# Kernel tuning notes

Hardware: AMD Instinct MI355X
Metric: run time of the kernel (lower is better)

Reference implementation:

```python
import jax, jax.numpy as jnp
import numpy as np

DIM = 768
NUM_HEADS = 12
HEAD_DIM = DIM // NUM_HEADS
ORDER_H = 8
RENORM = True
B, N = 4, 1024


def setup_inputs() -> dict:
    key = jax.random.key(0)
    ks = jax.random.split(key, 8)
    return {
        "x": jax.random.normal(ks[0], (B, N, DIM), dtype=jnp.float32),
        "qkv_w": jax.random.normal(ks[1], (3 * DIM, DIM), dtype=jnp.float32) * (DIM ** -0.5),
        "qkv_b": jax.random.normal(ks[2], (3 * DIM,), dtype=jnp.float32) * 0.02,
        "proj_w": jax.random.normal(ks[3], (DIM, DIM), dtype=jnp.float32) * (DIM ** -0.5),
        "proj_b": jax.random.normal(ks[4], (DIM,), dtype=jnp.float32) * 0.02,
        "lamb": jax.random.normal(ks[5], (NUM_HEADS,), dtype=jnp.float32) * 0.1,
        "gamma": 1.0 + jax.random.normal(ks[6], (NUM_HEADS,), dtype=jnp.float32) * 0.1,
        "delta": jax.random.normal(ks[7], (NUM_HEADS,), dtype=jnp.float32) * 0.1,
    }


def reference(x, qkv_w, qkv_b, proj_w, proj_b, lamb, gamma, delta):
    Bx, Nx, C = x.shape
    scale = HEAD_DIM ** -0.5
    # qkv: [B,N,3C] -> [3,B,H,N,hd]
    qkv = (x @ qkv_w.T + qkv_b).reshape(Bx, Nx, 3, NUM_HEADS, HEAD_DIM)
    qkv = jnp.transpose(qkv, (2, 0, 3, 1, 4))
    q, k, v = qkv[0], qkv[1], qkv[2]
    attn = jax.nn.softmax(jnp.einsum("bhid,bhjd->bhij", q, k) * scale, axis=-1)
    I = jnp.eye(Nx, dtype=attn.dtype)
    # GFSA high-order term: (h-1)*(A - I)@A + A
    high = (ORDER_H - 1) * jnp.einsum("bhik,bhkj->bhij", attn - I, attn) + attn
    beta_ = lamb[None, :, None, None]
    gamma_ = gamma[None, :, None, None]
    delta_ = delta[None, :, None, None]
    attn = delta_ * I + gamma_ * attn + beta_ * high
    if RENORM:
        attn = jnp.maximum(attn, 0.0)
        attn = attn / (attn.sum(axis=-1, keepdims=True) + 1e-9)
    out = jnp.einsum("bhij,bhjd->bhid", attn, v)  # [B,H,N,hd]
    out = jnp.transpose(out, (0, 2, 1, 3)).reshape(Bx, Nx, C)
    return out @ proj_w.T + proj_b
```

## Files before the change

### kernel.cpp

```cpp
#include <hip/hip_runtime.h>
#include <hip/hip_bf16.h>

#define DIMC 768
#define NH 12
#define HD 64
#define BB 4
#define NN 1024
#define BHT 48
#define QKVC 2304

typedef unsigned short u16;
typedef __attribute__((ext_vector_type(4))) unsigned short u16x4;
typedef __attribute__((ext_vector_type(8))) unsigned short u16x8;
typedef __attribute__((ext_vector_type(8))) short s16x8;
typedef __attribute__((ext_vector_type(4))) float f32x4;

#define GLD16(g, l) __builtin_amdgcn_global_load_lds( \
    (__attribute__((address_space(1))) void*)(g),     \
    (__attribute__((address_space(3))) void*)(l), 16, 0, 0)

__device__ __forceinline__ u16 f2bf(float f) {
    unsigned u = __float_as_uint(f);
    return (u16)((u + 0x7FFF + ((u >> 16) & 1)) >> 16);
}
__device__ __forceinline__ float bf2f(u16 v) {
    return __uint_as_float(((unsigned)v) << 16);
}
struct bfp { u16 h, l; };
__device__ __forceinline__ bfp splitf(float f) {
    bfp r;
    r.h = f2bf(f);
    r.l = f2bf(f - bf2f(r.h));
    return r;
}

__device__ __forceinline__ int swz_linear() {
    const int nwg = gridDim.x * gridDim.y * gridDim.z;
    const int L = blockIdx.x + gridDim.x * (blockIdx.y + gridDim.y * blockIdx.z);
    return (L & 7) * (nwg >> 3) + (L >> 3);
}

__global__ __launch_bounds__(256) void split_f2b(
    const float* __restrict__ src, u16* __restrict__ hi, u16* __restrict__ lo,
    int n4)
{
    int idx = blockIdx.x * 256 + threadIdx.x;
    if (idx >= n4) return;
    float4 v = *(const float4*)&src[idx * 4];
    u16x4 h, l;
    bfp s;
    s = splitf(v.x); h[0] = s.h; l[0] = s.l;
    s = splitf(v.y); h[1] = s.h; l[1] = s.l;
    s = splitf(v.z); h[2] = s.h; l[2] = s.l;
    s = splitf(v.w); h[3] = s.h; l[3] = s.l;
    *(u16x4*)&hi[idx * 4] = h;
    *(u16x4*)&lo[idx * 4] = l;
}

__global__ __launch_bounds__(256, 3) void gemm3_mfma(
    int Mrows, int Nout, int K,
    const u16* __restrict__ Ahp, const u16* __restrict__ Alp,
    const u16* __restrict__ Bhp, const u16* __restrict__ Blp,
    const float* __restrict__ bias, float* __restrict__ C)
{
    __shared__ alignas(16) u16 sAh[128 * 32], sAl[128 * 32], sBh[128 * 32], sBl[128 * 32];
    const int tid = threadIdx.x;
    const int W = swz_linear();
    const int j0 = (W % gridDim.x) * 128, i0 = (W / gridDim.x) * 128;
    const int w = tid >> 6, l = tid & 63;
    const int wr = w >> 1, wc = w & 1;
    const int l15 = l & 15, kb4 = l >> 4;
    const int lrow = l >> 2, lch = (l & 3) * 8;

    f32x4 acc[4][4];
    const f32x4 zero = {0.f, 0.f, 0.f, 0.f};
#pragma unroll
    for (int a = 0; a < 4; ++a)
#pragma unroll
        for (int b = 0; b < 4; ++b) acc[a][b] = zero;

    for (int k0 = 0; k0 < K; k0 += 32) {
#pragma unroll
        for (int t = 0; t < 2; ++t) {
            const int r = w * 32 + t * 16;
            const size_t ar = (size_t)(i0 + r + lrow) * K + k0 + lch;
            const size_t br = (size_t)(j0 + r + lrow) * K + k0 + lch;
            GLD16(&Ahp[ar], &sAh[r * 32]);
            GLD16(&Alp[ar], &sAl[r * 32]);
            GLD16(&Bhp[br], &sBh[r * 32]);
            GLD16(&Blp[br], &sBl[r * 32]);
        }
        __syncthreads();

        s16x8 ah[4], al[4], bh[4], bl[4];
#pragma unroll
        for (int f = 0; f < 4; ++f) {
            const int ao = (wr * 64 + f * 16 + l15) * 32 + kb4 * 8;
            const int bo = (wc * 64 + f * 16 + l15) * 32 + kb4 * 8;
            ah[f] = *(const s16x8*)&sAh[ao];
            al[f] = *(const s16x8*)&sAl[ao];
            bh[f] = *(const s16x8*)&sBh[bo];
            bl[f] = *(const s16x8*)&sBl[bo];
        }
#pragma unroll
        for (int fr = 0; fr < 4; ++fr)
#pragma unroll
            for (int fc = 0; fc < 4; ++fc) {
                acc[fr][fc] = __builtin_amdgcn_mfma_f32_16x16x32_bf16(
                    ah[fr], bh[fc], acc[fr][fc], 0, 0, 0);
                acc[fr][fc] = __builtin_amdgcn_mfma_f32_16x16x32_bf16(
                    ah[fr], bl[fc], acc[fr][fc], 0, 0, 0);
                acc[fr][fc] = __builtin_amdgcn_mfma_f32_16x16x32_bf16(
                    al[fr], bh[fc], acc[fr][fc], 0, 0, 0);
            }
        __syncthreads();
    }

#pragma unroll
    for (int fr = 0; fr < 4; ++fr)
#pragma unroll
        for (int r = 0; r < 4; ++r) {
            const int gi = i0 + wr * 64 + fr * 16 + kb4 * 4 + r;
#pragma unroll
            for (int fc = 0; fc < 4; ++fc) {
                const int gj = j0 + wc * 64 + fc * 16 + l15;
                C[(size_t)gi * Nout + gj] = acc[fr][fc][r] + bias[gj];
            }
        }
}

__global__ __launch_bounds__(256, 3) void qkv_fused_mfma(
    const u16* __restrict__ Ahp, const u16* __restrict__ Alp,
    const u16* __restrict__ Bhp, const u16* __restrict__ Blp,
    const float* __restrict__ bias,
    u16* __restrict__ qh, u16* __restrict__ ql,
    u16* __restrict__ kh, u16* __restrict__ kl,
    u16* __restrict__ vth, u16* __restrict__ vtl)
{
    __shared__ alignas(16) u16 sAh[128 * 32], sAl[128 * 32], sBh[128 * 32], sBl[128 * 32];
    const int tid = threadIdx.x;
    const int W = swz_linear();
    const int j0 = (W % gridDim.x) * 128, i0 = (W / gridDim.x) * 128;
    const int w = tid >> 6, l = tid & 63;
    const int wr = w >> 1, wc = w & 1;
    const int l15 = l & 15, kb4 = l >> 4;
    const int lrow = l >> 2, lch = (l & 3) * 8;
    const int K = DIMC;

    f32x4 acc[4][4];
    const f32x4 zero = {0.f, 0.f, 0.f, 0.f};
#pragma unroll
    for (int a = 0; a < 4; ++a)
#pragma unroll
        for (int b = 0; b < 4; ++b) acc[a][b] = zero;

    for (int k0 = 0; k0 < K; k0 += 32) {
#pragma unroll
        for (int t = 0; t < 2; ++t) {
            const int r = w * 32 + t * 16;
            const size_t ar = (size_t)(i0 + r + lrow) * K + k0 + lch;
            const size_t br = (size_t)(j0 + r + lrow) * K + k0 + lch;
            GLD16(&Ahp[ar], &sAh[r * 32]);
            GLD16(&Alp[ar], &sAl[r * 32]);
            GLD16(&Bhp[br], &sBh[r * 32]);
            GLD16(&Blp[br], &sBl[r * 32]);
        }
        __syncthreads();

        s16x8 ah[4], al[4], bh[4], bl[4];
#pragma unroll
        for (int f = 0; f < 4; ++f) {
            const int ao = (wr * 64 + f * 16 + l15) * 32 + kb4 * 8;
            const int bo = (wc * 64 + f * 16 + l15) * 32 + kb4 * 8;
            ah[f] = *(const s16x8*)&sAh[ao];
            al[f] = *(const s16x8*)&sAl[ao];
            bh[f] = *(const s16x8*)&sBh[bo];
            bl[f] = *(const s16x8*)&sBl[bo];
        }
#pragma unroll
        for (int fr = 0; fr < 4; ++fr)
#pragma unroll
            for (int fc = 0; fc < 4; ++fc) {
                acc[fr][fc] = __builtin_amdgcn_mfma_f32_16x16x32_bf16(
                    ah[fr], bh[fc], acc[fr][fc], 0, 0, 0);
                acc[fr][fc] = __builtin_amdgcn_mfma_f32_16x16x32_bf16(
                    ah[fr], bl[fc], acc[fr][fc], 0, 0, 0);
                acc[fr][fc] = __builtin_amdgcn_mfma_f32_16x16x32_bf16(
                    al[fr], bh[fc], acc[fr][fc], 0, 0, 0);
            }
        __syncthreads();
    }

    const int part = j0 / DIMC;
    const int hbase = (j0 % DIMC) >> 6;
    const int h = hbase + wc;

#pragma unroll
    for (int fr = 0; fr < 4; ++fr) {
        const int rowbase = i0 + wr * 64 + fr * 16 + kb4 * 4;
        const int b = rowbase >> 10;
        const int n0 = rowbase & 1023;
        const int bh = b * NH + h;
#pragma unroll
        for (int fc = 0; fc < 4; ++fc) {
            const int gj = j0 + wc * 64 + fc * 16 + l15;
            const float bv = bias[gj];
            const int d = fc * 16 + l15;
            if (part == 0) {
#pragma unroll
                for (int r = 0; r < 4; ++r) {
                    bfp s = splitf((acc[fr][fc][r] + bv) * 0.125f);
                    const size_t o = ((size_t)bh * NN + n0 + r) * HD + d;
                    qh[o] = s.h; ql[o] = s.l;
                }
            } else if (part == 1) {
#pragma unroll
                for (int r = 0; r < 4; ++r) {
                    bfp s = splitf(acc[fr][fc][r] + bv);
                    const size_t o = ((size_t)bh * NN + n0 + r) * HD + d;
                    kh[o] = s.h; kl[o] = s.l;
                }
            } else {
                u16x4 hv, lv;
#pragma unroll
                for (int r = 0; r < 4; ++r) {
                    bfp s = splitf(acc[fr][fc][r] + bv);
                    hv[r] = s.h; lv[r] = s.l;
                }
                const size_t o = ((size_t)bh * HD + d) * NN + n0;
                *(u16x4*)&vth[o] = hv;
                *(u16x4*)&vtl[o] = lv;
            }
        }
    }
}

__global__ __launch_bounds__(256, 4) void qk_mfma(
    const u16* __restrict__ qh, const u16* __restrict__ ql,
    const u16* __restrict__ kh, const u16* __restrict__ kl,
    float* __restrict__ Sb, int h0)
{
    __shared__ alignas(16) u16 sAh[128 * 32], sAl[128 * 32], sBh[128 * 32], sBl[128 * 32];
    const int tid = threadIdx.x;
    const int W = swz_linear();
    const int bhl = W >> 6;
    const int ib = W & 63;
    const int j0 = (ib & 7) * 128, i0 = (ib >> 3) * 128;
    const int bh = h0 + bhl;
    const int w = tid >> 6, l = tid & 63;
    const int wr = w >> 1, wc = w & 1;
    const int l15 = l & 15, kb4 = l >> 4;
    const int lrow = l >> 2, lch = (l & 3) * 8;

    f32x4 acc[4][4];
    const f32x4 zero = {0.f, 0.f, 0.f, 0.f};
#pragma unroll
    for (int a = 0; a < 4; ++a)
#pragma unroll
        for (int b = 0; b < 4; ++b) acc[a][b] = zero;

    for (int k0 = 0; k0 < HD; k0 += 32) {
#pragma unroll
        for (int t = 0; t < 2; ++t) {
            const int r = w * 32 + t * 16;
            const size_t ar = ((size_t)bh * NN + i0 + r + lrow) * HD + k0 + lch;
            const size_t br = ((size_t)bh * NN + j0 + r + lrow) * HD + k0 + lch;
            GLD16(&qh[ar], &sAh[r * 32]);
            GLD16(&ql[ar], &sAl[r * 32]);
            GLD16(&kh[br], &sBh[r * 32]);
            GLD16(&kl[br], &sBl[r * 32]);
        }
        __syncthreads();

        s16x8 ah[4], al[4], bh[4], bl[4];
#pragma unroll
        for (int f = 0; f < 4; ++f) {
            const int ao = (wr * 64 + f * 16 + l15) * 32 + kb4 * 8;
            const int bo = (wc * 64 + f * 16 + l15) * 32 + kb4 * 8;
            ah[f] = *(const s16x8*)&sAh[ao];
            al[f] = *(const s16x8*)&sAl[ao];
            bh[f] = *(const s16x8*)&sBh[bo];
            bl[f] = *(const s16x8*)&sBl[bo];
        }
#pragma unroll
        for (int fr = 0; fr < 4; ++fr)
#pragma unroll
            for (int fc = 0; fc < 4; ++fc) {
                acc[fr][fc] = __builtin_amdgcn_mfma_f32_16x16x32_bf16(
                    ah[fr], bh[fc], acc[fr][fc], 0, 0, 0);
                acc[fr][fc] = __builtin_amdgcn_mfma_f32_16x16x32_bf16(
                    ah[fr], bl[fc], acc[fr][fc], 0, 0, 0);
                acc[fr][fc] = __builtin_amdgcn_mfma_f32_16x16x32_bf16(
                    al[fr], bh[fc], acc[fr][fc], 0, 0, 0);
            }
        __syncthreads();
    }

    float* Sh = Sb + (size_t)bhl * NN * NN;
#pragma unroll
    for (int fr = 0; fr < 4; ++fr)
#pragma unroll
        for (int r = 0; r < 4; ++r) {
            const int gi = i0 + wr * 64 + fr * 16 + kb4 * 4 + r;
#pragma unroll
            for (int fc = 0; fc < 4; ++fc) {
                const int gj = j0 + wc * 64 + fc * 16 + l15;
                Sh[(size_t)gi * NN + gj] = acc[fr][fc][r];
            }
        }
}

__global__ __launch_bounds__(256) void softmax_w(
    const float* __restrict__ Sb, u16* __restrict__ Abf)
{
    const int w = threadIdx.x >> 6, l = threadIdx.x & 63;
    const int row = blockIdx.x * 4 + w;
    const float* p = Sb + (size_t)row * NN;
    u16* q = Abf + (size_t)row * NN;

    float4 v[4];
    float m = -1e30f;
#pragma unroll
    for (int c = 0; c < 4; ++c) {
        v[c] = *(const float4*)&p[c * 256 + l * 4];
        m = fmaxf(m, fmaxf(fmaxf(v[c].x, v[c].y), fmaxf(v[c].z, v[c].w)));
    }
#pragma unroll
    for (int off = 32; off >= 1; off >>= 1) m = fmaxf(m, __shfl_xor(m, off));

    float s = 0.f;
#pragma unroll
    for (int c = 0; c < 4; ++c) {
        v[c].x = expf(v[c].x - m); v[c].y = expf(v[c].y - m);
        v[c].z = expf(v[c].z - m); v[c].w = expf(v[c].w - m);
        s += v[c].x + v[c].y + v[c].z + v[c].w;
    }
#pragma unroll
    for (int off = 32; off >= 1; off >>= 1) s += __shfl_xor(s, off);

    const float inv = 1.0f / s;
#pragma unroll
    for (int c = 0; c < 4; ++c) {
        u16x4 o;
        o[0] = f2bf(v[c].x * inv); o[1] = f2bf(v[c].y * inv);
        o[2] = f2bf(v[c].z * inv); o[3] = f2bf(v[c].w * inv);
        *(u16x4*)&q[c * 256 + l * 4] = o;
    }
}

__global__ __launch_bounds__(256, 4) void mpow_mfma(
    const u16* __restrict__ Abf, u16* __restrict__ Mb,
    const float* __restrict__ lamb, const float* __restrict__ gamma,
    const float* __restrict__ delta, int h0)
{
    __shared__ alignas(16) u16 sA[128 * 64], sB[128 * 64];
    const int tid = threadIdx.x;
    const int W = swz_linear();
    const int bz = W >> 6;
    const int ib = W & 63;
    const int j0 = (ib & 7) * 128, i0 = (ib >> 3) * 128;
    const int h = (h0 + bz) % NH;
    const u16* Ah = Abf + (size_t)bz * NN * NN;

    const int w = tid >> 6, l = tid & 63;
    const int wr = w >> 1, wc = w & 1;
    const int l15 = l & 15, kb4 = l >> 4;
    const int lr8 = l >> 3;
    const int srck = ((l & 7) ^ lr8) * 8;
    const int kr = tid & 31;
    const int jc = (tid >> 5) * 16;

    f32x4 acc[4][4];
    const f32x4 zero = {0.f, 0.f, 0.f, 0.f};
#pragma unroll
    for (int a = 0; a < 4; ++a)
#pragma unroll
        for (int b = 0; b < 4; ++b) acc[a][b] = zero;

    for (int k0 = 0; k0 < NN; k0 += 64) {
#pragma unroll
        for (int t = 0; t < 4; ++t) {
            const int r = w * 32 + t * 8;
            GLD16(&Ah[(size_t)(i0 + r + lr8) * NN + k0 + srck], &sA[r * 64]);
        }
#pragma unroll
        for (int kk2 = 0; kk2 < 64; kk2 += 32) {
            const int kloc = kk2 + kr;
            const u16* arow = &Ah[(size_t)(k0 + kloc) * NN + j0 + jc];
            u16x8 b0 = *(const u16x8*)arow;
            u16x8 b1 = *(const u16x8*)(arow + 8);
            const int kc = kloc >> 3, ke = kloc & 7;
#pragma unroll
            for (int e = 0; e < 8; ++e) {
                const int j1 = jc + e, j2 = jc + 8 + e;
                sB[j1 * 64 + ((kc ^ (j1 & 7)) * 8) + ke] = b0[e];
                sB[j2 * 64 + ((kc ^ (j2 & 7)) * 8) + ke] = b1[e];
            }
        }
        __syncthreads();

#pragma unroll
        for (int kk = 0; kk < 64; kk += 32) {
            const int ck = kk >> 3;
            s16x8 af[4], bf[4];
#pragma unroll
            for (int f = 0; f < 4; ++f) {
                const int ar_ = wr * 64 + f * 16 + l15;
                const int br_ = wc * 64 + f * 16 + l15;
                af[f] = *(const s16x8*)&sA[ar_ * 64 + (((ck + kb4) ^ (ar_ & 7)) * 8)];
                bf[f] = *(const s16x8*)&sB[br_ * 64 + (((ck + kb4) ^ (br_ & 7)) * 8)];
            }
#pragma unroll
            for (int fr = 0; fr < 4; ++fr)
#pragma unroll
                for (int fc = 0; fc < 4; ++fc)
                    acc[fr][fc] = __builtin_amdgcn_mfma_f32_16x16x32_bf16(
                        af[fr], bf[fc], acc[fr][fc], 0, 0, 0);
        }
        __syncthreads();
    }

    const float lam = lamb[h];
    const float c1 = gamma[h] - 6.0f * lam;
    const float c2 = 7.0f * lam;
    const float del = delta[h];
    u16* Mh = Mb + (size_t)bz * NN * NN;

#pragma unroll
    for (int fr = 0; fr < 4; ++fr)
#pragma unroll
        for (int r = 0; r < 4; ++r) {
            const int gi = i0 + wr * 64 + fr * 16 + kb4 * 4 + r;
#pragma unroll
            for (int fc = 0; fc < 4; ++fc) {
                const int gj = j0 + wc * 64 + fc * 16 + l15;
                const float a = bf2f(Ah[(size_t)gi * NN + gj]);
                float m = c2 * acc[fr][fc][r] + c1 * a + (gi == gj ? del : 0.f);
                m = fmaxf(m, 0.f);
                Mh[(size_t)gi * NN + gj] = f2bf(m);
            }
        }
}

__global__ __launch_bounds__(256, 4) void pv_mfma(
    const u16* __restrict__ Mb,
    const u16* __restrict__ vth, const u16* __restrict__ vtl,
    u16* __restrict__ aoh, u16* __restrict__ aol, int h0)
{
    __shared__ alignas(16) u16 sM[64 * 32], sVh[64 * 32], sVl[64 * 32];
    const int tid = threadIdx.x;
    const int W = swz_linear();
    const int bhl = W >> 4;
    const int i0 = (W & 15) * 64;
    const int bh = h0 + bhl;
    const int b = bh / NH, h = bh % NH;
    const u16* Mh = Mb + (size_t)bhl * NN * NN;
    const u16* vhb = vth + (size_t)bh * HD * NN;
    const u16* vlb = vtl + (size_t)bh * HD * NN;

    const int w = tid >> 6, l = tid & 63;
    const int l15 = l & 15, kb4 = l >> 4;
    const int lrow = l >> 2, lch = (l & 3) * 8;

    f32x4 acc[4], accs;
    const f32x4 zero = {0.f, 0.f, 0.f, 0.f};
#pragma unroll
    for (int c = 0; c < 4; ++c) acc[c] = zero;
    accs = zero;
    s16x8 ones;
#pragma unroll
    for (int e = 0; e < 8; ++e) ones[e] = (short)0x3F80;

    for (int k0 = 0; k0 < NN; k0 += 32) {
        {
            const int r = w * 16;
            GLD16(&Mh[(size_t)(i0 + r + lrow) * NN + k0 + lch], &sM[r * 32]);
            const size_t vr = (size_t)(r + lrow) * NN + k0 + lch;
            GLD16(&vhb[vr], &sVh[r * 32]);
            GLD16(&vlb[vr], &sVl[r * 32]);
        }
        __syncthreads();

        s16x8 af, bh[4], bl[4];
        af = *(const s16x8*)&sM[(w * 16 + l15) * 32 + kb4 * 8];
#pragma unroll
        for (int f = 0; f < 4; ++f) {
            bh[f] = *(const s16x8*)&sVh[(f * 16 + l15) * 32 + kb4 * 8];
            bl[f] = *(const s16x8*)&sVl[(f * 16 + l15) * 32 + kb4 * 8];
        }
#pragma unroll
        for (int fc = 0; fc < 4; ++fc) {
            acc[fc] = __builtin_amdgcn_mfma_f32_16x16x32_bf16(
                af, bh[fc], acc[fc], 0, 0, 0);
            acc[fc] = __builtin_amdgcn_mfma_f32_16x16x32_bf16(
                af, bl[fc], acc[fc], 0, 0, 0);
        }
        accs = __builtin_amdgcn_mfma_f32_16x16x32_bf16(af, ones, accs, 0, 0, 0);
        __syncthreads();
    }

#pragma unroll
    for (int r = 0; r < 4; ++r) {
        const int gi = i0 + w * 16 + kb4 * 4 + r;
        const float inv = 1.0f / (accs[r] + 1e-9f);
        const size_t ob = (size_t)(b * NN + gi) * DIMC + h * HD;
#pragma unroll
        for (int fc = 0; fc < 4; ++fc) {
            const int gd = fc * 16 + l15;
            bfp s = splitf(acc[fc][r] * inv);
            aoh[ob + gd] = s.h;
            aol[ob + gd] = s.l;
        }
    }
}

extern "C" void kernel_launch(void* const* d_in, const int* in_sizes, int n_in,
                              void* d_out, int out_size, void* d_ws, size_t ws_size,
                              hipStream_t stream)
{
    const float* x      = (const float*)d_in[0];
    const float* qkv_w  = (const float*)d_in[1];
    const float* qkv_b  = (const float*)d_in[2];
    const float* proj_w = (const float*)d_in[3];
    const float* proj_b = (const float*)d_in[4];
    const float* lamb   = (const float*)d_in[5];
    const float* gamma  = (const float*)d_in[6];
    const float* delta  = (const float*)d_in[7];

    char* p = (char*)d_ws;
    u16* xh  = (u16*)p;                     p += (size_t)4096 * DIMC * 2;
    u16* xl  = (u16*)p;                     p += (size_t)4096 * DIMC * 2;
    u16* wh  = (u16*)p;                     p += (size_t)QKVC * DIMC * 2;
    u16* wl  = (u16*)p;                     p += (size_t)QKVC * DIMC * 2;
    u16* pwh = (u16*)p;                     p += (size_t)DIMC * DIMC * 2;
    u16* pwl = (u16*)p;                     p += (size_t)DIMC * DIMC * 2;
    u16* qh  = (u16*)p;                     p += (size_t)BHT * NN * HD * 2;
    u16* ql  = (u16*)p;                     p += (size_t)BHT * NN * HD * 2;
    u16* kh  = (u16*)p;                     p += (size_t)BHT * NN * HD * 2;
    u16* kl  = (u16*)p;                     p += (size_t)BHT * NN * HD * 2;
    u16* vth = (u16*)p;                     p += (size_t)BHT * HD * NN * 2;
    u16* vtl = (u16*)p;                     p += (size_t)BHT * HD * NN * 2;
    u16* aoh = (u16*)p;                     p += (size_t)4096 * DIMC * 2;
    u16* aol = (u16*)p;                     p += (size_t)4096 * DIMC * 2;
    const size_t fixed = (size_t)(p - (char*)d_ws);

    const size_t perh = (size_t)NN * NN * 4 + (size_t)NN * NN * 2;
    static const int choices[] = {48, 24, 16, 12, 8, 6, 4, 3, 2, 1};
    int CH = 1;
    for (int ci = 0; ci < 10; ++ci) {
        int c = choices[ci];
        if (fixed + (size_t)c * perh <= ws_size) { CH = c; break; }
    }

    float* Sb = (float*)p;                  p += (size_t)CH * NN * NN * 4;
    u16* Abf  = (u16*)p;                    p += (size_t)CH * NN * NN * 2;
    u16* Mb   = (u16*)Sb;

    split_f2b<<<dim3((4096 * DIMC / 4 + 255) / 256), 256, 0, stream>>>(x, xh, xl, 4096 * DIMC / 4);
    split_f2b<<<dim3((QKVC * DIMC / 4 + 255) / 256), 256, 0, stream>>>(qkv_w, wh, wl, QKVC * DIMC / 4);
    split_f2b<<<dim3((DIMC * DIMC / 4 + 255) / 256), 256, 0, stream>>>(proj_w, pwh, pwl, DIMC * DIMC / 4);

    qkv_fused_mfma<<<dim3(QKVC / 128, 4096 / 128), 256, 0, stream>>>(
        xh, xl, wh, wl, qkv_b, qh, ql, kh, kl, vth, vtl);

    for (int h0 = 0; h0 < BHT; h0 += CH) {
        qk_mfma<<<dim3(8, 8, CH), 256, 0, stream>>>(qh, ql, kh, kl, Sb, h0);
        softmax_w<<<dim3(CH * NN / 4), 256, 0, stream>>>(Sb, Abf);
        mpow_mfma<<<dim3(8, 8, CH), 256, 0, stream>>>(
            Abf, Mb, lamb, gamma, delta, h0);
        pv_mfma<<<dim3(16, CH), 256, 0, stream>>>(Mb, vth, vtl, aoh, aol, h0);
    }

    gemm3_mfma<<<dim3(DIMC / 128, 4096 / 128), 256, 0, stream>>>(
        4096, DIMC, DIMC, aoh, aol, pwh, pwl, proj_b, (float*)d_out);
}
```

Baseline: 401.4 us.

## Pre-transpose attention matrix so A@A loads both operands via direct LDS copies

Adds a separate kernel that writes a transposed bf16 copy of the softmaxed attention matrix. The A@A kernel can then stream both operands with global_load_lds instead of scattering per-element transposed stores into shared memory. The k-step also drops from 64 to 32, halving LDS tiles and removing the XOR swizzle. In exchange it costs an extra full NxN read and write per head, a larger workspace per head that may shrink the chunk count, and possible LDS bank conflicts without the swizzle.

```diff
diff --git a/kernel.cpp b/kernel.cpp
--- a/kernel.cpp
+++ b/kernel.cpp
@@ -348,12 +348,42 @@
     }
 }
 
+__global__ __launch_bounds__(256) void transpose_b2b(
+    const u16* __restrict__ src0, u16* __restrict__ dst0)
+{
+    __shared__ u16 t[64][65];
+    const int tid = threadIdx.x;
+    const int j0 = blockIdx.x * 64, i0 = blockIdx.y * 64;
+    const int bz = blockIdx.z;
+    const u16* src = src0 + (size_t)bz * NN * NN;
+    u16* dst = dst0 + (size_t)bz * NN * NN;
+
+    const int row = tid >> 2, ch = tid & 3;
+    const size_t sp = (size_t)(i0 + row) * NN + j0 + ch * 16;
+    u16x8 v0 = *(const u16x8*)&src[sp];
+    u16x8 v1 = *(const u16x8*)&src[sp + 8];
+#pragma unroll
+    for (int e = 0; e < 8; ++e) { t[row][ch * 16 + e] = v0[e]; t[row][ch * 16 + 8 + e] = v1[e]; }
+    __syncthreads();
+
+    const int oj = tid >> 2, och = tid & 3;
+    u16x8 o0, o1;
+#pragma unroll
+    for (int e = 0; e < 8; ++e) o0[e] = t[och * 16 + e][oj];
+#pragma unroll
+    for (int e = 0; e < 8; ++e) o1[e] = t[och * 16 + 8 + e][oj];
+    const size_t dp = (size_t)(j0 + oj) * NN + i0 + och * 16;
+    *(u16x8*)&dst[dp] = o0;
+    *(u16x8*)&dst[dp + 8] = o1;
+}
+
 __global__ __launch_bounds__(256, 4) void mpow_mfma(
-    const u16* __restrict__ Abf, u16* __restrict__ Mb,
+    const u16* __restrict__ Abf, const u16* __restrict__ Atb,
+    u16* __restrict__ Mb,
     const float* __restrict__ lamb, const float* __restrict__ gamma,
     const float* __restrict__ delta, int h0)
 {
-    __shared__ alignas(16) u16 sA[128 * 64], sB[128 * 64];
+    __shared__ alignas(16) u16 sA[128 * 32], sB[128 * 32];
     const int tid = threadIdx.x;
     const int W = swz_linear();
     const int bz = W >> 6;
@@ -361,14 +391,12 @@
     const int j0 = (ib & 7) * 128, i0 = (ib >> 3) * 128;
     const int h = (h0 + bz) % NH;
     const u16* Ah = Abf + (size_t)bz * NN * NN;
+    const u16* Ath = Atb + (size_t)bz * NN * NN;
 
     const int w = tid >> 6, l = tid & 63;
     const int wr = w >> 1, wc = w & 1;
     const int l15 = l & 15, kb4 = l >> 4;
-    const int lr8 = l >> 3;
-    const int srck = ((l & 7) ^ lr8) * 8;
-    const int kr = tid & 31;
-    const int jc = (tid >> 5) * 16;
+    const int lrow = l >> 2, lch = (l & 3) * 8;
 
     f32x4 acc[4][4];
     const f32x4 zero = {0.f, 0.f, 0.f, 0.f};
@@ -377,46 +405,27 @@
 #pragma unroll
         for (int b = 0; b < 4; ++b) acc[a][b] = zero;
 
-    for (int k0 = 0; k0 < NN; k0 += 64) {
-#pragma unroll
-        for (int t = 0; t < 4; ++t) {
-            const int r = w * 32 + t * 8;
-            GLD16(&Ah[(size_t)(i0 + r + lr8) * NN + k0 + srck], &sA[r * 64]);
-        }
-#pragma unroll
-        for (int kk2 = 0; kk2 < 64; kk2 += 32) {
-            const int kloc = kk2 + kr;
-            const u16* arow = &Ah[(size_t)(k0 + kloc) * NN + j0 + jc];
-            u16x8 b0 = *(const u16x8*)arow;
-            u16x8 b1 = *(const u16x8*)(arow + 8);
-            const int kc = kloc >> 3, ke = kloc & 7;
-#pragma unroll
-            for (int e = 0; e < 8; ++e) {
-                const int j1 = jc + e, j2 = jc + 8 + e;
-                sB[j1 * 64 + ((kc ^ (j1 & 7)) * 8) + ke] = b0[e];
-                sB[j2 * 64 + ((kc ^ (j2 & 7)) * 8) + ke] = b1[e];
-            }
-        }
-        __syncthreads();
-
-#pragma unroll
-        for (int kk = 0; kk < 64; kk += 32) {
-            const int ck = kk >> 3;
-            s16x8 af[4], bf[4];
-#pragma unroll
-            for (int f = 0; f < 4; ++f) {
-                const int ar_ = wr * 64 + f * 16 + l15;
-                const int br_ = wc * 64 + f * 16 + l15;
-                af[f] = *(const s16x8*)&sA[ar_ * 64 + (((ck + kb4) ^ (ar_ & 7)) * 8)];
-                bf[f] = *(const s16x8*)&sB[br_ * 64 + (((ck + kb4) ^ (br_ & 7)) * 8)];
-            }
-#pragma unroll
-            for (int fr = 0; fr < 4; ++fr)
-#pragma unroll
-                for (int fc = 0; fc < 4; ++fc)
-                    acc[fr][fc] = __builtin_amdgcn_mfma_f32_16x16x32_bf16(
-                        af[fr], bf[fc], acc[fr][fc], 0, 0, 0);
-        }
+    for (int k0 = 0; k0 < NN; k0 += 32) {
+#pragma unroll
+        for (int t = 0; t < 2; ++t) {
+            const int r = w * 32 + t * 16;
+            GLD16(&Ah[(size_t)(i0 + r + lrow) * NN + k0 + lch], &sA[r * 32]);
+            GLD16(&Ath[(size_t)(j0 + r + lrow) * NN + k0 + lch], &sB[r * 32]);
+        }
+        __syncthreads();
+
+        s16x8 af[4], bf[4];
+#pragma unroll
+        for (int f = 0; f < 4; ++f) {
+            af[f] = *(const s16x8*)&sA[(wr * 64 + f * 16 + l15) * 32 + kb4 * 8];
+            bf[f] = *(const s16x8*)&sB[(wc * 64 + f * 16 + l15) * 32 + kb4 * 8];
+        }
+#pragma unroll
+        for (int fr = 0; fr < 4; ++fr)
+#pragma unroll
+            for (int fc = 0; fc < 4; ++fc)
+                acc[fr][fc] = __builtin_amdgcn_mfma_f32_16x16x32_bf16(
+                    af[fr], bf[fc], acc[fr][fc], 0, 0, 0);
         __syncthreads();
     }
 
@@ -544,7 +553,7 @@
     u16* aol = (u16*)p;                     p += (size_t)4096 * DIMC * 2;
     const size_t fixed = (size_t)(p - (char*)d_ws);
 
-    const size_t perh = (size_t)NN * NN * 4 + (size_t)NN * NN * 2;
+    const size_t perh = (size_t)NN * NN * 4 + 2 * (size_t)NN * NN * 2;
     static const int choices[] = {48, 24, 16, 12, 8, 6, 4, 3, 2, 1};
     int CH = 1;
     for (int ci = 0; ci < 10; ++ci) {
@@ -554,6 +563,7 @@
 
     float* Sb = (float*)p;                  p += (size_t)CH * NN * NN * 4;
     u16* Abf  = (u16*)p;                    p += (size_t)CH * NN * NN * 2;
+    u16* Atb  = (u16*)p;                    p += (size_t)CH * NN * NN * 2;
     u16* Mb   = (u16*)Sb;
 
     split_f2b<<<dim3((4096 * DIMC / 4 + 255) / 256), 256, 0, stream>>>(x, xh, xl, 4096 * DIMC / 4);
@@ -566,8 +576,9 @@
     for (int h0 = 0; h0 < BHT; h0 += CH) {
         qk_mfma<<<dim3(8, 8, CH), 256, 0, stream>>>(qh, ql, kh, kl, Sb, h0);
         softmax_w<<<dim3(CH * NN / 4), 256, 0, stream>>>(Sb, Abf);
+        transpose_b2b<<<dim3(16, 16, CH), 256, 0, stream>>>(Abf, Atb);
         mpow_mfma<<<dim3(8, 8, CH), 256, 0, stream>>>(
-            Abf, Mb, lamb, gamma, delta, h0);
+            Abf, Atb, Mb, lamb, gamma, delta, h0);
         pv_mfma<<<dim3(16, CH), 256, 0, stream>>>(Mb, vth, vtl, aoh, aol, h0);
     }
 
```

Measured after the change: 453.4 us. 1.13x slower.
